# Optimization experiments

Measured on AMD Instinct MI355X. Metric: run time of the kernel, lower is better.

Reference implementation:

```python
import jax, jax.numpy as jnp
import numpy as np

B, CIN, H, W = 8, 32, 64, 64  # x1/x2 each 32 ch; concat -> 64
C = 2 * CIN


def setup_inputs() -> dict:
    key = jax.random.key(0)
    ks = jax.random.split(key, 8)
    s = 0.05
    return {
        "x1": jax.random.normal(ks[0], (B, CIN, H, W), jnp.float32),
        "x2": jax.random.normal(ks[1], (B, CIN, H, W), jnp.float32),
        "Wq": jax.random.normal(ks[2], (C // 2, C), jnp.float32) * s,
        "bq": jax.random.normal(ks[3], (C // 2,), jnp.float32) * s,
        "Wk": jax.random.normal(ks[4], (C // 2, C), jnp.float32) * s,
        "bk": jax.random.normal(ks[5], (C // 2,), jnp.float32) * s,
        "Wv": jax.random.normal(ks[6], (C, C), jnp.float32) * s,
        "Wsc": jax.random.normal(ks[7], (C // 2, C), jnp.float32) * s,
        "gamma": jnp.array([0.5], jnp.float32),
    }


def reference(x1, x2, Wq, bq, Wk, bk, Wv, Wsc, gamma):
    x = jnp.concatenate([x1, x2], axis=1)  # [b, c, h, w]
    b, c, h, w = x.shape
    hw = h * w
    # 1x1 convs == per-pixel linear projections
    q = (jnp.einsum('oc,bchw->bohw', Wq, x) + bq[None, :, None, None]).reshape(b, c // 2, hw)
    q = q.transpose(0, 2, 1)  # [b, hw, c/2]
    k = (jnp.einsum('oc,bchw->bohw', Wk, x) + bk[None, :, None, None]).reshape(b, c // 2, hw)
    am = jnp.einsum('bnd,bdm->bnm', q, k)  # [b, hw, hw]
    a = jax.nn.softmax(am, axis=1)  # softmax over dim=1 (queries axis) as in the torch code
    v = jnp.einsum('oc,bchw->bohw', Wv, x).reshape(b, c, hw)  # [b, c, hw]
    # out = bmm(v, a^T): out[b,c,n] = sum_m v[b,c,m] * a[b,n,m]
    out = jnp.einsum('bcm,bnm->bcn', v, a).reshape(b, c, h, w)
    out = gamma[0] * out + x
    out = jnp.einsum('oc,bchw->bohw', Wsc, out)  # [b, c/2, h, w]
    return out
```

## Files before the change

kernel.cpp:

```cpp
#include <hip/hip_runtime.h>

typedef __attribute__((ext_vector_type(8))) __bf16 bf16x8;
typedef __attribute__((ext_vector_type(4))) float f32x4;
typedef unsigned int uint32;

#define HW   4096
#define CCH  64
#define DQ   32
#define OC   32
#define LOG2E 1.4426950408889634f

#define WSV_OFF  0u
#define QB_OFF   2048u
#define KB_OFF   (QB_OFF + 524288u)
#define XS_OFF   (KB_OFF + 524288u)
#define V2_OFF   (XS_OFF + 1048576u)
#define ZP_OFF   (V2_OFF + 1048576u)
#define VZB_OFF  (ZP_OFF + 262144u)
#define OUTP_OFF (VZB_OFF + 524288u)

__device__ __forceinline__ uint32 f2bf(float x) {
    uint32 u = __builtin_bit_cast(uint32, x);
    return (u + 0x7fffu + ((u >> 16) & 1u)) >> 16;
}
__device__ __forceinline__ uint32 packbf(float a, float b) {
    return f2bf(a) | (f2bf(b) << 16);
}
__device__ __forceinline__ uint32 packbf_t(float a, float b) {
    return __builtin_amdgcn_perm(__builtin_bit_cast(uint32, b),
                                 __builtin_bit_cast(uint32, a), 0x07060302u);
}
__device__ __forceinline__ bf16x8 ldfrag(const unsigned short* p) {
    union { uint4 u; bf16x8 f; } t;
    t.u = *(const uint4*)p;
    return t.f;
}
__device__ __forceinline__ float fexp2(float x) {
#if __has_builtin(__builtin_amdgcn_exp2f)
    return __builtin_amdgcn_exp2f(x);
#else
    return __expf(x * 0.6931471805599453f);
#endif
}

__global__ __launch_bounds__(256) void k_wcomb(const float* __restrict__ Wsc,
                                               const float* __restrict__ Wv,
                                               float* __restrict__ Wsv) {
    int t = blockIdx.x * 256 + threadIdx.x;
    if (t < OC * CCH) {
        int o = t / CCH, ci = t % CCH;
        float s = 0.f;
        #pragma unroll
        for (int c = 0; c < CCH; ++c) s += Wsc[o * CCH + c] * Wv[c * CCH + ci];
        Wsv[t] = s;
    }
}

__global__ __launch_bounds__(256) void k_proj(
    const float* __restrict__ x1, const float* __restrict__ x2,
    const float* __restrict__ Wq, const float* __restrict__ bq,
    const float* __restrict__ Wk, const float* __restrict__ bk,
    const float* __restrict__ Wsv, const float* __restrict__ Wsc,
    unsigned short* __restrict__ qb, unsigned short* __restrict__ kb,
    float* __restrict__ v2, float* __restrict__ xs) {
    int t = threadIdx.x;
    int g = __builtin_amdgcn_readfirstlane(t >> 6);
    int l = t & 63;
    int p = blockIdx.x * 64 + l;
    int b = p >> 12, n = p & 4095;
    const float* x1b = x1 + (size_t)b * 32 * HW + n;
    const float* x2b = x2 + (size_t)b * 32 * HW + n;
    float x[CCH];
    #pragma unroll
    for (int c = 0; c < 32; ++c) x[c] = x1b[(size_t)c * HW];
    #pragma unroll
    for (int c = 0; c < 32; ++c) x[32 + c] = x2b[(size_t)c * HW];

    if (g < 2) {
        const float* W    = g ? Wk : Wq;
        const float* bias = g ? bk : bq;
        float scale = g ? 1.0f : LOG2E;
        unsigned short* dst = g ? kb : qb;
        size_t row = ((size_t)b * HW + n) * DQ;
        for (int d0 = 0; d0 < DQ; d0 += 8) {
            float r[8];
            #pragma unroll
            for (int i = 0; i < 8; ++i) {
                const float* wr = W + (d0 + i) * CCH;
                float a = bias[d0 + i];
                #pragma unroll
                for (int c = 0; c < CCH; ++c) a += wr[c] * x[c];
                r[i] = a * scale;
            }
            uint4 u;
            u.x = packbf(r[0], r[1]); u.y = packbf(r[2], r[3]);
            u.z = packbf(r[4], r[5]); u.w = packbf(r[6], r[7]);
            *(uint4*)(dst + row + d0) = u;
        }
    } else {
        const float* W = (g == 2) ? Wsv : Wsc;
        float* dst     = (g == 2) ? v2  : xs;
        for (int o = 0; o < OC; ++o) {
            const float* wr = W + o * CCH;
            float a = 0.f;
            #pragma unroll
            for (int c = 0; c < CCH; ++c) a += wr[c] * x[c];
            dst[((size_t)b * OC + o) * HW + n] = a;
        }
    }
}

__global__ __launch_bounds__(256, 8) void k_stats(
    const unsigned short* __restrict__ kb, const unsigned short* __restrict__ qb,
    float* __restrict__ zp) {
    int t = threadIdx.x;
    int w = t >> 6, l = t & 63;
    int lr = l & 15, lq = l >> 4;
    int bid = blockIdx.x;
    int b = bid & 7, nc = (bid >> 3) & 7, mg = bid >> 6;
    int m0 = mg * 128 + w * 32;

    const unsigned short* kbb = kb + ((size_t)b * HW) * DQ;
    bf16x8 af0 = ldfrag(kbb + (size_t)(m0 + lr) * DQ + lq * 8);
    bf16x8 af1 = ldfrag(kbb + (size_t)(m0 + 16 + lr) * DQ + lq * 8);
    const unsigned short* qp = qb + ((size_t)b * HW + nc * 512 + lr) * DQ + lq * 8;

    f32x4 acc0 = {0.f, 0.f, 0.f, 0.f};
    f32x4 acc1 = {0.f, 0.f, 0.f, 0.f};
    f32x4 zz = {0.f, 0.f, 0.f, 0.f};
    #pragma unroll 4
    for (int i = 0; i < 32; ++i) {
        bf16x8 qf = ldfrag(qp);
        qp += 16 * DQ;
        f32x4 s0 = __builtin_amdgcn_mfma_f32_16x16x32_bf16(af0, qf, zz, 0, 0, 0);
        f32x4 s1 = __builtin_amdgcn_mfma_f32_16x16x32_bf16(af1, qf, zz, 0, 0, 0);
        acc0.x += fexp2(s0.x); acc0.y += fexp2(s0.y);
        acc0.z += fexp2(s0.z); acc0.w += fexp2(s0.w);
        acc1.x += fexp2(s1.x); acc1.y += fexp2(s1.y);
        acc1.z += fexp2(s1.z); acc1.w += fexp2(s1.w);
    }
    #pragma unroll
    for (int off = 1; off < 16; off <<= 1) {
        acc0.x += __shfl_xor(acc0.x, off); acc0.y += __shfl_xor(acc0.y, off);
        acc0.z += __shfl_xor(acc0.z, off); acc0.w += __shfl_xor(acc0.w, off);
        acc1.x += __shfl_xor(acc1.x, off); acc1.y += __shfl_xor(acc1.y, off);
        acc1.z += __shfl_xor(acc1.z, off); acc1.w += __shfl_xor(acc1.w, off);
    }
    if (lr == 0) {
        size_t base = (size_t)nc * 32768 + (size_t)b * HW;
        zp[base + m0 + lq * 4 + 0] = acc0.x;
        zp[base + m0 + lq * 4 + 1] = acc0.y;
        zp[base + m0 + lq * 4 + 2] = acc0.z;
        zp[base + m0 + lq * 4 + 3] = acc0.w;
        zp[base + m0 + 16 + lq * 4 + 0] = acc1.x;
        zp[base + m0 + 16 + lq * 4 + 1] = acc1.y;
        zp[base + m0 + 16 + lq * 4 + 2] = acc1.z;
        zp[base + m0 + 16 + lq * 4 + 3] = acc1.w;
    }
}

__global__ __launch_bounds__(256) void k_zvz(const float* __restrict__ zp,
                                             const float* __restrict__ v2,
                                             const float* __restrict__ gamma,
                                             unsigned short* __restrict__ vzb) {
    int i = blockIdx.x * 256 + threadIdx.x;
    float s = 0.f;
    #pragma unroll
    for (int nc = 0; nc < 8; ++nc) s += zp[nc * 32768 + i];
    float zs = gamma[0] / s;
    int b = i >> 12, m = i & 4095;
    const float* vsrc = v2 + ((size_t)b * OC) * HW + m;
    unsigned short* dst = vzb + ((size_t)b * OC) * HW + m;
    #pragma unroll 8
    for (int o = 0; o < OC; ++o) {
        dst[(size_t)o * HW] = (unsigned short)f2bf(vsrc[(size_t)o * HW] * zs);
    }
}

__global__ __launch_bounds__(256, 8) void k_attn(
    const unsigned short* __restrict__ qb, const unsigned short* __restrict__ kb,
    const unsigned short* __restrict__ vzb, unsigned short* __restrict__ outp) {
    __shared__ unsigned short fb[8192];
    int t = threadIdx.x;
    int w = t >> 6, l = t & 63;
    int lr = l & 15, lq = l >> 4;
    int bid = blockIdx.x;
    int b = bid & 7, mc = (bid >> 3) & 7, ng = bid >> 6;
    int nA = ng * 128 + w * 32;

    unsigned short* fbw = fb + w * 2048;
    int aw = (lr + ((lq >> 1) << 4)) * 8 + (lq & 1) * 4;

    bf16x8 qfA = ldfrag(qb + ((size_t)b * HW + nA + lr) * DQ + lq * 8);
    bf16x8 qfB = ldfrag(qb + ((size_t)b * HW + nA + 16 + lr) * DQ + lq * 8);
    const unsigned short* kp = kb + ((size_t)b * HW + lr) * DQ + lq * 8;
    const unsigned short* vp = vzb + ((size_t)b * OC + lr) * HW + lq * 8;

    f32x4 accA0 = {0.f,0.f,0.f,0.f}, accA1 = {0.f,0.f,0.f,0.f};
    f32x4 accB0 = {0.f,0.f,0.f,0.f}, accB1 = {0.f,0.f,0.f,0.f};
    f32x4 zz = {0.f,0.f,0.f,0.f};

    int mbeg = mc * 512;
    for (int m0 = mbeg; m0 < mbeg + 512; m0 += 64) {
        #pragma unroll
        for (int ph = 0; ph < 2; ++ph) {
            int mb = m0 + ph * 32;
            unsigned short* fA = fbw + ph * 512;
            unsigned short* fB = fbw + 1024 + ph * 512;
            bf16x8 a0  = ldfrag(kp + (size_t)mb * DQ);
            bf16x8 a1  = ldfrag(kp + (size_t)(mb + 16) * DQ);
            bf16x8 va0 = ldfrag(vp + mb);
            bf16x8 va1 = ldfrag(vp + 16 * HW + mb);
            f32x4 sA0 = __builtin_amdgcn_mfma_f32_16x16x32_bf16(a0, qfA, zz, 0, 0, 0);
            f32x4 sA1 = __builtin_amdgcn_mfma_f32_16x16x32_bf16(a1, qfA, zz, 0, 0, 0);
            f32x4 sB0 = __builtin_amdgcn_mfma_f32_16x16x32_bf16(a0, qfB, zz, 0, 0, 0);
            f32x4 sB1 = __builtin_amdgcn_mfma_f32_16x16x32_bf16(a1, qfB, zz, 0, 0, 0);
            uint2 pA0, pA1, pB0, pB1;
            pA0.x = packbf_t(fexp2(sA0.x), fexp2(sA0.y));
            pA0.y = packbf_t(fexp2(sA0.z), fexp2(sA0.w));
            pA1.x = packbf_t(fexp2(sA1.x), fexp2(sA1.y));
            pA1.y = packbf_t(fexp2(sA1.z), fexp2(sA1.w));
            pB0.x = packbf_t(fexp2(sB0.x), fexp2(sB0.y));
            pB0.y = packbf_t(fexp2(sB0.z), fexp2(sB0.w));
            pB1.x = packbf_t(fexp2(sB1.x), fexp2(sB1.y));
            pB1.y = packbf_t(fexp2(sB1.z), fexp2(sB1.w));
            *(uint2*)(fA + aw)       = pA0;
            *(uint2*)(fA + aw + 256) = pA1;
            *(uint2*)(fB + aw)       = pB0;
            *(uint2*)(fB + aw + 256) = pB1;
            bf16x8 pfA = ldfrag(fA + l * 8);
            bf16x8 pfB = ldfrag(fB + l * 8);
            accA0 = __builtin_amdgcn_mfma_f32_16x16x32_bf16(va0, pfA, accA0, 0, 0, 0);
            accA1 = __builtin_amdgcn_mfma_f32_16x16x32_bf16(va1, pfA, accA1, 0, 0, 0);
            accB0 = __builtin_amdgcn_mfma_f32_16x16x32_bf16(va0, pfB, accB0, 0, 0, 0);
            accB1 = __builtin_amdgcn_mfma_f32_16x16x32_bf16(va1, pfB, accB1, 0, 0, 0);
        }
    }

    int n_A = nA + lr, n_B = nA + 16 + lr;
    unsigned short* ob = outp + ((size_t)(mc * 8 + b) * OC) * HW;
    #pragma unroll
    for (int r = 0; r < 4; ++r) {
        int o0 = lq * 4 + r;
        ob[(size_t)o0 * HW + n_A]        = (unsigned short)f2bf(accA0[r]);
        ob[(size_t)(o0 + 16) * HW + n_A] = (unsigned short)f2bf(accA1[r]);
        ob[(size_t)o0 * HW + n_B]        = (unsigned short)f2bf(accB0[r]);
        ob[(size_t)(o0 + 16) * HW + n_B] = (unsigned short)f2bf(accB1[r]);
    }
}

__global__ __launch_bounds__(256) void k_red(const unsigned short* __restrict__ outp,
                                             const float* __restrict__ xs,
                                             float* __restrict__ out) {
    int i = (blockIdx.x * 256 + threadIdx.x) * 4;
    float4 r = *(const float4*)(xs + i);
    const unsigned short* op = outp + i;
    #pragma unroll
    for (int mc = 0; mc < 8; ++mc) {
        uint2 p = *(const uint2*)(op + (size_t)mc * 1048576);
        r.x += __builtin_bit_cast(float, p.x << 16);
        r.y += __builtin_bit_cast(float, p.x & 0xffff0000u);
        r.z += __builtin_bit_cast(float, p.y << 16);
        r.w += __builtin_bit_cast(float, p.y & 0xffff0000u);
    }
    *(float4*)(out + i) = r;
}

extern "C" void kernel_launch(void* const* d_in, const int* in_sizes, int n_in,
                              void* d_out, int out_size, void* d_ws, size_t ws_size,
                              hipStream_t stream) {
    const float* x1    = (const float*)d_in[0];
    const float* x2    = (const float*)d_in[1];
    const float* Wq    = (const float*)d_in[2];
    const float* bq    = (const float*)d_in[3];
    const float* Wk    = (const float*)d_in[4];
    const float* bk    = (const float*)d_in[5];
    const float* Wv    = (const float*)d_in[6];
    const float* Wsc   = (const float*)d_in[7];
    const float* gamma = (const float*)d_in[8];
    float* out = (float*)d_out;
    float* ws  = (float*)d_ws;

    float*          wsv  = ws + WSV_OFF;
    unsigned short* qbp  = (unsigned short*)(ws + QB_OFF);
    unsigned short* kbp  = (unsigned short*)(ws + KB_OFF);
    float*          xsp  = ws + XS_OFF;
    float*          v2   = ws + V2_OFF;
    float*          zpp  = ws + ZP_OFF;
    unsigned short* vzb  = (unsigned short*)(ws + VZB_OFF);
    unsigned short* outp = (unsigned short*)(ws + OUTP_OFF);

    k_wcomb<<<8, 256, 0, stream>>>(Wsc, Wv, wsv);
    k_proj<<<512, 256, 0, stream>>>(x1, x2, Wq, bq, Wk, bk, wsv, Wsc,
                                    qbp, kbp, v2, xsp);
    k_stats<<<2048, 256, 0, stream>>>(kbp, qbp, zpp);
    k_zvz<<<128, 256, 0, stream>>>(zpp, v2, gamma, vzb);
    k_attn<<<2048, 256, 0, stream>>>(qbp, kbp, vzb, outp);
    k_red<<<1024, 256, 0, stream>>>(outp, xsp, out);
}
```

Before: 179.5 us.

## Feed exp scores directly into fp16 MFMA, removing LDS round-trip in attention

The attention loop now computes scores with one bf16 MFMA per 16-key chunk and feeds the exponentiated, fp16-packed results straight into 16x16x16 fp16 MFMAs. The per-warp shared-memory scratch used to re-layout probabilities is dropped, because the output layout of the first MFMA already matches the B operand of the second. V*z is stored as fp16 instead of bf16 to match. This removes LDS stores and loads and their latency, but uses the smaller-K MFMA (more instructions per key) and round-toward-zero fp16 conversion, which can overflow if exp values exceed fp16 range.

```diff
diff --git a/kernel.cpp b/kernel.cpp
--- a/kernel.cpp
+++ b/kernel.cpp
@@ -2,6 +2,7 @@
 
 typedef __attribute__((ext_vector_type(8))) __bf16 bf16x8;
 typedef __attribute__((ext_vector_type(4))) float f32x4;
+typedef _Float16 f16x4 __attribute__((ext_vector_type(4)));
 typedef unsigned int uint32;
 
 #define HW   4096
@@ -26,13 +27,20 @@
 __device__ __forceinline__ uint32 packbf(float a, float b) {
     return f2bf(a) | (f2bf(b) << 16);
 }
-__device__ __forceinline__ uint32 packbf_t(float a, float b) {
-    return __builtin_amdgcn_perm(__builtin_bit_cast(uint32, b),
-                                 __builtin_bit_cast(uint32, a), 0x07060302u);
-}
 __device__ __forceinline__ bf16x8 ldfrag(const unsigned short* p) {
     union { uint4 u; bf16x8 f; } t;
     t.u = *(const uint4*)p;
+    return t.f;
+}
+__device__ __forceinline__ f16x4 ldv4h(const unsigned short* p) {
+    union { uint2 u; f16x4 f; } t;
+    t.u = *(const uint2*)p;
+    return t.f;
+}
+__device__ __forceinline__ f16x4 pk4(float a, float b, float c, float d) {
+    union { uint2 u; f16x4 f; } t;
+    t.u.x = __builtin_bit_cast(uint32, __builtin_amdgcn_cvt_pkrtz(a, b));
+    t.u.y = __builtin_bit_cast(uint32, __builtin_amdgcn_cvt_pkrtz(c, d));
     return t.f;
 }
 __device__ __forceinline__ float fexp2(float x) {
@@ -173,14 +181,14 @@
     unsigned short* dst = vzb + ((size_t)b * OC) * HW + m;
     #pragma unroll 8
     for (int o = 0; o < OC; ++o) {
-        dst[(size_t)o * HW] = (unsigned short)f2bf(vsrc[(size_t)o * HW] * zs);
+        _Float16 h = (_Float16)(vsrc[(size_t)o * HW] * zs);
+        dst[(size_t)o * HW] = __builtin_bit_cast(unsigned short, h);
     }
 }
 
 __global__ __launch_bounds__(256, 8) void k_attn(
     const unsigned short* __restrict__ qb, const unsigned short* __restrict__ kb,
     const unsigned short* __restrict__ vzb, unsigned short* __restrict__ outp) {
-    __shared__ unsigned short fb[8192];
     int t = threadIdx.x;
     int w = t >> 6, l = t & 63;
     int lr = l & 15, lq = l >> 4;
@@ -188,52 +196,31 @@
     int b = bid & 7, mc = (bid >> 3) & 7, ng = bid >> 6;
     int nA = ng * 128 + w * 32;
 
-    unsigned short* fbw = fb + w * 2048;
-    int aw = (lr + ((lq >> 1) << 4)) * 8 + (lq & 1) * 4;
-
     bf16x8 qfA = ldfrag(qb + ((size_t)b * HW + nA + lr) * DQ + lq * 8);
     bf16x8 qfB = ldfrag(qb + ((size_t)b * HW + nA + 16 + lr) * DQ + lq * 8);
     const unsigned short* kp = kb + ((size_t)b * HW + lr) * DQ + lq * 8;
-    const unsigned short* vp = vzb + ((size_t)b * OC + lr) * HW + lq * 8;
+    const unsigned short* vp = vzb + ((size_t)b * OC + lr) * HW + lq * 4;
 
     f32x4 accA0 = {0.f,0.f,0.f,0.f}, accA1 = {0.f,0.f,0.f,0.f};
     f32x4 accB0 = {0.f,0.f,0.f,0.f}, accB1 = {0.f,0.f,0.f,0.f};
     f32x4 zz = {0.f,0.f,0.f,0.f};
 
     int mbeg = mc * 512;
-    for (int m0 = mbeg; m0 < mbeg + 512; m0 += 64) {
+    for (int m0 = mbeg; m0 < mbeg + 512; m0 += 32) {
         #pragma unroll
         for (int ph = 0; ph < 2; ++ph) {
-            int mb = m0 + ph * 32;
-            unsigned short* fA = fbw + ph * 512;
-            unsigned short* fB = fbw + 1024 + ph * 512;
-            bf16x8 a0  = ldfrag(kp + (size_t)mb * DQ);
-            bf16x8 a1  = ldfrag(kp + (size_t)(mb + 16) * DQ);
-            bf16x8 va0 = ldfrag(vp + mb);
-            bf16x8 va1 = ldfrag(vp + 16 * HW + mb);
-            f32x4 sA0 = __builtin_amdgcn_mfma_f32_16x16x32_bf16(a0, qfA, zz, 0, 0, 0);
-            f32x4 sA1 = __builtin_amdgcn_mfma_f32_16x16x32_bf16(a1, qfA, zz, 0, 0, 0);
-            f32x4 sB0 = __builtin_amdgcn_mfma_f32_16x16x32_bf16(a0, qfB, zz, 0, 0, 0);
-            f32x4 sB1 = __builtin_amdgcn_mfma_f32_16x16x32_bf16(a1, qfB, zz, 0, 0, 0);
-            uint2 pA0, pA1, pB0, pB1;
-            pA0.x = packbf_t(fexp2(sA0.x), fexp2(sA0.y));
-            pA0.y = packbf_t(fexp2(sA0.z), fexp2(sA0.w));
-            pA1.x = packbf_t(fexp2(sA1.x), fexp2(sA1.y));
-            pA1.y = packbf_t(fexp2(sA1.z), fexp2(sA1.w));
-            pB0.x = packbf_t(fexp2(sB0.x), fexp2(sB0.y));
-            pB0.y = packbf_t(fexp2(sB0.z), fexp2(sB0.w));
-            pB1.x = packbf_t(fexp2(sB1.x), fexp2(sB1.y));
-            pB1.y = packbf_t(fexp2(sB1.z), fexp2(sB1.w));
-            *(uint2*)(fA + aw)       = pA0;
-            *(uint2*)(fA + aw + 256) = pA1;
-            *(uint2*)(fB + aw)       = pB0;
-            *(uint2*)(fB + aw + 256) = pB1;
-            bf16x8 pfA = ldfrag(fA + l * 8);
-            bf16x8 pfB = ldfrag(fB + l * 8);
-            accA0 = __builtin_amdgcn_mfma_f32_16x16x32_bf16(va0, pfA, accA0, 0, 0, 0);
-            accA1 = __builtin_amdgcn_mfma_f32_16x16x32_bf16(va1, pfA, accA1, 0, 0, 0);
-            accB0 = __builtin_amdgcn_mfma_f32_16x16x32_bf16(va0, pfB, accB0, 0, 0, 0);
-            accB1 = __builtin_amdgcn_mfma_f32_16x16x32_bf16(va1, pfB, accB1, 0, 0, 0);
+            int mb = m0 + ph * 16;
+            bf16x8 a   = ldfrag(kp + (size_t)mb * DQ);
+            f16x4  va0 = ldv4h(vp + mb);
+            f16x4  va1 = ldv4h(vp + (size_t)16 * HW + mb);
+            f32x4 sA = __builtin_amdgcn_mfma_f32_16x16x32_bf16(a, qfA, zz, 0, 0, 0);
+            f32x4 sB = __builtin_amdgcn_mfma_f32_16x16x32_bf16(a, qfB, zz, 0, 0, 0);
+            f16x4 pA = pk4(fexp2(sA.x), fexp2(sA.y), fexp2(sA.z), fexp2(sA.w));
+            f16x4 pB = pk4(fexp2(sB.x), fexp2(sB.y), fexp2(sB.z), fexp2(sB.w));
+            accA0 = __builtin_amdgcn_mfma_f32_16x16x16f16(va0, pA, accA0, 0, 0, 0);
+            accA1 = __builtin_amdgcn_mfma_f32_16x16x16f16(va1, pA, accA1, 0, 0, 0);
+            accB0 = __builtin_amdgcn_mfma_f32_16x16x16f16(va0, pB, accB0, 0, 0, 0);
+            accB1 = __builtin_amdgcn_mfma_f32_16x16x16f16(va1, pB, accB1, 0, 0, 0);
         }
     }
 
```

Measured after the change: 209.1 us. 1.16x slower.
